# Kernel optimization log

Measured on AMD Instinct MI355X. Metric: run time of the kernel, lower is better.

Reference implementation:

```python
import jax, jax.numpy as jnp
import numpy as np

INV_L_MIN, INV_L_MAX = 0.5, 2.0

def _gelu(v):
    return jax.nn.gelu(v, approximate=False)  # torch F.gelu default = exact erf

def compute_gradient(f, directed_edges, edge_gradient_weights):
    # f: [b, c, n] ; directed_edges: [b, e, 2] (target, source) ; egw: [b, e, d]
    f = jnp.transpose(f, (0, 2, 1))                      # [b, n, c]
    b, n, c = f.shape
    e, d = edge_gradient_weights.shape[1], edge_gradient_weights.shape[2]
    target, source = directed_edges[..., 0], directed_edges[..., 1]
    fs = jnp.take_along_axis(f, source[:, :, None], axis=1)   # [b, e, c]
    ft = jnp.take_along_axis(f, target[:, :, None], axis=1)   # [b, e, c]
    # einsum('bed,bec->becd') then reshape -> channel-major (c*d) layout
    msg = (edge_gradient_weights[:, :, None, :] * (fs - ft)[:, :, :, None]).reshape(b, e, c * d)
    seg = (target + n * jnp.arange(b, dtype=target.dtype)[:, None]).reshape(-1)
    grad = jax.ops.segment_sum(msg.reshape(b * e, c * d), seg, num_segments=b * n)
    return jnp.transpose(grad.reshape(b, n, c * d), (0, 2, 1))  # [b, c*d, n]

def spectral_conv(x, wc, ws_, w0, bc, bs, b0, wbc, wbs, wb0):
    # x: [b, c, n]; bases: [b, n, k, w]; weights: [c, o, k, w]
    xc = jnp.einsum('bcx,bxkw->bckw', x, wbc)
    xs = jnp.einsum('bcx,bxkw->bckw', x, wbs)
    x0 = jnp.einsum('bcx,bxkw->bckw', x, wb0)
    fc = jnp.einsum('bckw,cokw->bokw', xc, wc) - jnp.einsum('bckw,cokw->bokw', xs, ws_)
    fs = jnp.einsum('bckw,cokw->bokw', xs, wc) + jnp.einsum('bckw,cokw->bokw', xc, ws_)
    f0 = jnp.einsum('bckw,cokw->bokw', x0, w0)
    return (jnp.einsum('bokw,bxkw->box', f0, b0)
            + 2 * jnp.einsum('bokw,bxkw->box', fc, bc)
            - 2 * jnp.einsum('bokw,bxkw->box', fs, bs))

def setup_inputs():
    key = jax.random.key(0)
    ks = jax.random.split(key, 16)
    B, N, E = 4, 20000, 100000
    NDIMS, NMEAS, NMODES = 3, 1, 32
    C, L = 128, 3
    IN_DIM, FC_DIM, OUT_DIM = 3, 128, 1
    f32 = jnp.float32
    inp = {}
    inp['x'] = jax.random.normal(ks[0], (B, N, IN_DIM), f32)
    inp['node_mask'] = jnp.ones((B, N, 1), jnp.int32)
    inp['nodes'] = jax.random.uniform(ks[1], (B, N, NDIMS), f32)
    inp['node_weights'] = jax.random.uniform(ks[2], (B, N, NMEAS), f32) / N
    inp['directed_edges'] = jax.random.randint(ks[3], (B, E, 2), 0, N, jnp.int32)
    inp['edge_gradient_weights'] = jax.random.normal(ks[4], (B, E, NDIMS), f32)
    # modes k = 2*pi*K/L0, K integer-like
    inp['modes'] = (2 * jnp.pi * jax.random.randint(ks[5], (NMODES, NDIMS, NMEAS), 1, 9)).astype(f32)
    # scaled_logit(1.0, 0.5, 2.0): sigmoid(l)=1/3 -> l=log(0.5)
    inp['inv_L_scale_latent'] = jnp.full((NDIMS, NMEAS), np.log(0.5), f32)
    inp['fc0_w'] = jax.random.normal(ks[6], (C, IN_DIM), f32) / np.sqrt(IN_DIM)
    inp['fc0_b'] = jnp.zeros((C,), f32)
    sc = 1.0 / (C * C)
    inp['swc'] = sc * jax.random.uniform(ks[7], (L, C, C, NMODES, NMEAS), f32)
    inp['sws'] = sc * jax.random.uniform(ks[8], (L, C, C, NMODES, NMEAS), f32)
    inp['sw0'] = sc * jax.random.uniform(ks[9], (L, C, C, 1, NMEAS), f32)
    inp['ww'] = jax.random.normal(ks[10], (L, C, C), f32) / np.sqrt(C)
    inp['wb'] = jnp.zeros((L, C), f32)
    inp['gw'] = jax.random.normal(ks[11], (L, C, NDIMS * C), f32) / np.sqrt(NDIMS * C)
    inp['gb'] = jnp.zeros((L, C), f32)
    inp['fc1_w'] = jax.random.normal(ks[12], (FC_DIM, C), f32) / np.sqrt(C)
    inp['fc1_b'] = jnp.zeros((FC_DIM,), f32)
    inp['fc2_w'] = jax.random.normal(ks[13], (OUT_DIM, FC_DIM), f32) / np.sqrt(FC_DIM)
    inp['fc2_b'] = jnp.zeros((OUT_DIM,), f32)
    return inp

def reference(x, node_mask, nodes, node_weights, directed_edges, edge_gradient_weights,
              modes, inv_L_scale_latent, fc0_w, fc0_b, swc, sws, sw0, ww, wb, gw, gb,
              fc1_w, fc1_b, fc2_w, fc2_b):
    inv_L = INV_L_MIN + (INV_L_MAX - INV_L_MIN) * jax.nn.sigmoid(inv_L_scale_latent)  # [d, w]
    t = jnp.einsum('bxd,kdw->bxkw', nodes, modes * inv_L[None])
    bc, bs = jnp.cos(t), jnp.sin(t)
    b0 = jnp.ones(t.shape[:2] + (1, t.shape[3]), t.dtype)
    w = node_weights[:, :, None, :]
    wbc, wbs, wb0 = bc * w, bs * w, b0 * w
    h = jnp.einsum('bni,ci->bnc', x, fc0_w) + fc0_b        # lift
    h = jnp.transpose(h, (0, 2, 1))                        # [b, C, n]
    L = swc.shape[0]
    for i in range(L):
        h1 = spectral_conv(h, swc[i], sws[i], sw0[i], bc, bs, b0, wbc, wbs, wb0)
        h2 = jnp.einsum('oc,bcn->bon', ww[i], h) + wb[i][None, :, None]
        g = compute_gradient(h, directed_edges, edge_gradient_weights)
        h3 = jnp.einsum('oc,bcn->bon', gw[i], g) + gb[i][None, :, None]
        h = h1 + h2 + h3
        if i != L - 1:
            h = _gelu(h)
    h = jnp.transpose(h, (0, 2, 1))                        # [b, n, C]
    h = _gelu(h @ fc1_w.T + fc1_b)
    return h @ fc2_w.T + fc2_b                             # [b, n, out_dim]
```

## Files before the change

### kernel.cpp

```cpp
#include <hip/hip_runtime.h>
#include <math.h>

#define B_ 4
#define N_ 20000
#define E_ 100000
#define C_ 128
#define K_ 32
#define NPAD 20480
#define NROWS (B_*N_ + 128)

typedef __attribute__((ext_vector_type(8))) short short8;
typedef __attribute__((ext_vector_type(4))) float floatx4;
typedef __attribute__((ext_vector_type(4))) unsigned int uintx4;
typedef __attribute__((ext_vector_type(2))) unsigned int uintx2;

__device__ __forceinline__ float gelu_exact(float x){
    return 0.5f * x * (1.0f + erff(x * 0.70710678118654752f));
}

__device__ __forceinline__ unsigned short f2bf(float f){
    unsigned int u = __builtin_bit_cast(unsigned int, f);
    u += 0x7FFFu + ((u >> 16) & 1u);
    return (unsigned short)(u >> 16);
}
__device__ __forceinline__ unsigned int pack2(float a, float b){
    return (unsigned int)f2bf(a) | ((unsigned int)f2bf(b) << 16);
}
__device__ __forceinline__ float bf2f(unsigned short u){
    unsigned int v = ((unsigned int)u) << 16;
    return __builtin_bit_cast(float, v);
}
__device__ __forceinline__ float u2f(unsigned int u){
    return __builtin_bit_cast(float, u);
}

#define WAITV(n) asm volatile("s_waitcnt vmcnt(" #n ")" ::: "memory")
#define BAR() __builtin_amdgcn_s_barrier()


__global__ __launch_bounds__(256) void basis_kernel(
    const float* __restrict__ nodes, const float* __restrict__ nw,
    const float* __restrict__ modes, const float* __restrict__ latent,
    unsigned short* __restrict__ bcb, unsigned short* __restrict__ bsb,
    unsigned short* __restrict__ wBt)
{
    __shared__ float lx[64], ly[64], lz[64], lwv[64];
    __shared__ unsigned short lTc[32*64], lTs[32*64];
    int b = blockIdx.y, n0 = blockIdx.x*64;
    int tid = threadIdx.x;
    size_t bN = (size_t)b*N_;
    if (tid < 64){
        int n = n0 + tid;
        float iL0 = 0.5f + 1.5f/(1.f+expf(-latent[0]));
        float iL1 = 0.5f + 1.5f/(1.f+expf(-latent[1]));
        float iL2 = 0.5f + 1.5f/(1.f+expf(-latent[2]));
        if (n < N_){
            lx[tid] = nodes[(bN+n)*3+0]*iL0;
            ly[tid] = nodes[(bN+n)*3+1]*iL1;
            lz[tid] = nodes[(bN+n)*3+2]*iL2;
            lwv[tid] = nw[bN+n];
        } else { lx[tid]=0.f; ly[tid]=0.f; lz[tid]=0.f; lwv[tid]=0.f; }
    }
    __syncthreads();
    int node = tid>>2, k0 = (tid&3)*8;
    float p0 = lx[node], p1 = ly[node], p2 = lz[node], w = lwv[node];
    float cv[8], sv[8];
    #pragma unroll
    for (int i=0;i<8;i++){
        int k = k0+i;
        float t = p0*modes[k*3+0] + p1*modes[k*3+1] + p2*modes[k*3+2];
        cv[i] = cosf(t); sv[i] = sinf(t);
        lTc[k*64 + node] = f2bf(w*cv[i]);
        lTs[k*64 + node] = f2bf(w*sv[i]);
    }
    int gn = n0 + node;
    if (gn < N_){
        uintx4 uc = (uintx4){pack2(cv[0],cv[1]), pack2(cv[2],cv[3]),
                             pack2(cv[4],cv[5]), pack2(cv[6],cv[7])};
        uintx4 us = (uintx4){pack2(sv[0],sv[1]), pack2(sv[2],sv[3]),
                             pack2(sv[4],sv[5]), pack2(sv[6],sv[7])};
        *(uintx4*)&bcb[(bN+gn)*K_ + k0] = uc;
        *(uintx4*)&bsb[(bN+gn)*K_ + k0] = us;
    }
    __syncthreads();
    #pragma unroll
    for (int i=0;i<5;i++){
        int idx = i*256 + tid;
        int row = idx>>4, seg = idx&15;
        unsigned short v0,v1,v2,v3;
        if (row < 32){
            v0=lTc[row*64+seg*4+0]; v1=lTc[row*64+seg*4+1];
            v2=lTc[row*64+seg*4+2]; v3=lTc[row*64+seg*4+3];
        } else if (row < 64){
            int r = row-32;
            v0=lTs[r*64+seg*4+0]; v1=lTs[r*64+seg*4+1];
            v2=lTs[r*64+seg*4+2]; v3=lTs[r*64+seg*4+3];
        } else if (row == 64){
            v0=f2bf(lwv[seg*4+0]); v1=f2bf(lwv[seg*4+1]);
            v2=f2bf(lwv[seg*4+2]); v3=f2bf(lwv[seg*4+3]);
        } else { v0=v1=v2=v3=0; }
        uintx2 u;
        u.x = (unsigned int)v0 | ((unsigned int)v1<<16);
        u.y = (unsigned int)v2 | ((unsigned int)v3<<16);
        *(uintx2*)&wBt[((size_t)b*80+row)*NPAD + n0 + seg*4] = u;
    }
}


__global__ __launch_bounds__(256) void fc0_kernel(
    const float* __restrict__ x, const float* __restrict__ w,
    const float* __restrict__ bvec, unsigned short* __restrict__ hN,
    unsigned short* __restrict__ hT)
{
    int idx = blockIdx.x*256 + threadIdx.x;
    if (idx >= B_*NPAD) return;
    int b = idx / NPAD, n = idx - b*NPAD;
    if (n >= N_){
        for (int c=0;c<C_;c++)
            hT[((size_t)b*C_+c)*NPAD + n] = 0;
        return;
    }
    size_t idn = (size_t)b*N_ + n;
    float x0 = x[idn*3+0], x1 = x[idn*3+1], x2 = x[idn*3+2];
    unsigned short* hr = hN + idn*C_;
    for (int c=0;c<C_;c+=4){
        float4 v;
        v.x = bvec[c+0] + x0*w[(c+0)*3] + x1*w[(c+0)*3+1] + x2*w[(c+0)*3+2];
        v.y = bvec[c+1] + x0*w[(c+1)*3] + x1*w[(c+1)*3+1] + x2*w[(c+1)*3+2];
        v.z = bvec[c+2] + x0*w[(c+2)*3] + x1*w[(c+2)*3+1] + x2*w[(c+2)*3+2];
        v.w = bvec[c+3] + x0*w[(c+3)*3] + x1*w[(c+3)*3+1] + x2*w[(c+3)*3+2];
        uintx2 u; u.x = pack2(v.x,v.y); u.y = pack2(v.z,v.w);
        *(uintx2*)(hr+c) = u;
        hT[((size_t)b*C_+c+0)*NPAD + n] = f2bf(v.x);
        hT[((size_t)b*C_+c+1)*NPAD + n] = f2bf(v.y);
        hT[((size_t)b*C_+c+2)*NPAD + n] = f2bf(v.z);
        hT[((size_t)b*C_+c+3)*NPAD + n] = f2bf(v.w);
    }
}


__global__ __launch_bounds__(256) void hist_kernel(
    const int* __restrict__ edges, int* __restrict__ cnt)
{
    int idx = blockIdx.x*256 + threadIdx.x;
    if (idx >= B_*E_) return;
    int b = idx / E_;
    int t = edges[(size_t)idx*2];
    atomicAdd(cnt + b*N_ + t, 1);
}

__global__ __launch_bounds__(1024) void scan_kernel(
    const int* __restrict__ cnt, int* __restrict__ rowptr, int* __restrict__ cur)
{
    __shared__ int wsum[16];
    int b = blockIdx.x, tid = threadIdx.x;
    int lane = tid & 63, wv = tid >> 6;
    const int CHUNK = 20;
    int start = tid * CHUNK;
    int lc[CHUNK];
    int lsum = 0;
    #pragma unroll
    for (int i=0;i<CHUNK;i++){
        int n = start + i;
        int v = (n < N_) ? cnt[b*N_+n] : 0;
        lc[i] = v; lsum += v;
    }
    int v = lsum;
    #pragma unroll
    for (int off=1; off<64; off<<=1){
        int t = __shfl_up(v, off, 64);
        if (lane >= off) v += t;
    }
    if (lane == 63) wsum[wv] = v;
    __syncthreads();
    if (wv == 0 && lane < 16){
        int wv2 = wsum[lane];
        #pragma unroll
        for (int off=1; off<16; off<<=1){
            int t = __shfl_up(wv2, off, 64);
            if (lane >= off) wv2 += t;
        }
        wsum[lane] = wv2;
    }
    __syncthreads();
    int waveoff = (wv == 0) ? 0 : wsum[wv-1];
    int excl = waveoff + v - lsum;
    #pragma unroll
    for (int i=0;i<CHUNK;i++){
        int n = start + i;
        if (n < N_){
            rowptr[b*(N_+1)+n] = excl;
            cur[b*N_+n] = excl;
            excl += lc[i];
        }
    }
    if (tid == 0) rowptr[b*(N_+1)+N_] = E_;
}

__global__ __launch_bounds__(256) void fill_kernel(
    const int* __restrict__ edges, const float* __restrict__ egw,
    int* __restrict__ cur, uintx4* __restrict__ epack)
{
    int idx = blockIdx.x*256 + threadIdx.x;
    if (idx >= B_*E_) return;
    int b = idx / E_;
    int t = edges[(size_t)idx*2];
    int src = edges[(size_t)idx*2+1];
    uintx4 rec;
    rec.x = (unsigned int)src;
    rec.y = __builtin_bit_cast(unsigned int, egw[(size_t)idx*3+0]);
    rec.z = __builtin_bit_cast(unsigned int, egw[(size_t)idx*3+1]);
    rec.w = __builtin_bit_cast(unsigned int, egw[(size_t)idx*3+2]);
    int pos = atomicAdd(cur + b*N_ + t, 1);
    epack[(size_t)b*E_ + pos] = rec;
}


__global__ __launch_bounds__(256) void wconv_kernel(
    const float* __restrict__ ww, const float* __restrict__ gw,
    unsigned short* __restrict__ wcat3)
{
    int o = blockIdx.x, l = blockIdx.y, t = threadIdx.x;
    const float* ww_l = ww + (size_t)l*C_*C_;
    const float* gw_l = gw + (size_t)l*C_*C_*3;
    int k = t*2;
    float a, bv;
    if (k < 128){ a = ww_l[(size_t)o*C_ + k];      bv = ww_l[(size_t)o*C_ + k + 1]; }
    else        { a = gw_l[(size_t)o*384 + k-128]; bv = gw_l[(size_t)o*384 + k-127]; }
    *(unsigned int*)&wcat3[((size_t)l*C_ + o)*512 + k] = pack2(a, bv);
}

__global__ __launch_bounds__(64) void fc1conv_kernel(
    const float* __restrict__ fc1w, unsigned short* __restrict__ w16)
{
    int o = blockIdx.x, t = threadIdx.x;
    int k = t*2;
    *(unsigned int*)&w16[(size_t)o*C_ + k] = pack2(fc1w[(size_t)o*C_+k], fc1w[(size_t)o*C_+k+1]);
}


__global__ __launch_bounds__(256) void stageA_kernel(
    const unsigned short* __restrict__ hT, const unsigned short* __restrict__ wBt,
    float* __restrict__ part)
{
    __shared__ unsigned short stg[2][160*64];
    int b = blockIdx.y;
    int blk = blockIdx.x >> 1;
    int half = blockIdx.x & 1;
    int tid = threadIdx.x;
    int wv = tid>>6, lane = tid&63, l15 = lane&15, quad = lane>>4;
    floatx4 acc[5];
    #pragma unroll
    for (int mt=0;mt<5;mt++) acc[mt]=(floatx4){0,0,0,0};
    size_t hbase = (size_t)b*C_*NPAD;
    size_t wbase = (size_t)b*80*NPAD;
    int n0 = blk*320;
    const unsigned short* sp[5];
    #pragma unroll
    for (int q=0;q<5;q++){
        int li = q*256 + tid;
        int r = li>>3;
        int u = (li&7) ^ (r&7);
        int rw = (r < 80) ? r : 79;
        sp[q] = (r < 96) ? (wBt + wbase + (size_t)rw*NPAD + n0 + u*8)
                         : (hT  + hbase + (size_t)(half*64 + r-96)*NPAD + n0 + u*8);
    }

#define SSTG(ch) do{ \
    _Pragma("unroll") \
    for (int q=0;q<5;q++) \
        __builtin_amdgcn_global_load_lds( \
            (const __attribute__((address_space(1))) void*)(sp[q] + (ch)*64), \
            (__attribute__((address_space(3))) void*)&stg[(ch)&1][q*2048 + wv*512], \
            16, 0, 0); }while(0)

#define SCOMP(ch) do{ \
    __builtin_amdgcn_s_setprio(1); \
    _Pragma("unroll") \
    for (int ks=0; ks<2; ks++){ \
        short8 bfrag = *(const short8*)&stg[(ch)&1][(96 + wv*16 + l15)*64 + (((ks*4+quad)^(l15&7))*8)]; \
        _Pragma("unroll") \
        for (int mt=0;mt<5;mt++){ \
            short8 af = *(const short8*)&stg[(ch)&1][(mt*16+l15)*64 + (((ks*4+quad)^(l15&7))*8)]; \
            acc[mt] = __builtin_amdgcn_mfma_f32_16x16x32_bf16(af, bfrag, acc[mt], 0,0,0); \
        } } \
    __builtin_amdgcn_s_setprio(0); }while(0)

    SSTG(0); SSTG(1);
    WAITV(5); BAR(); SCOMP(0); BAR(); SSTG(2);
    WAITV(5); BAR(); SCOMP(1); BAR(); SSTG(3);
    WAITV(5); BAR(); SCOMP(2); BAR(); SSTG(4);
    WAITV(5); BAR(); SCOMP(3);
    WAITV(0); BAR(); SCOMP(4);
#undef SSTG
#undef SCOMP

    float* pblk = part + ((size_t)(b*64+blk))*80*C_;
    int cg = half*64 + wv*16 + l15;
    #pragma unroll
    for (int mt=0;mt<5;mt++){
        #pragma unroll
        for (int r=0;r<4;r++){
            int kcol = mt*16 + quad*4 + r;
            pblk[kcol*C_ + cg] = acc[mt][r];
        }
    }
}

__global__ __launch_bounds__(256) void reducePart_kernel(
    const float* __restrict__ part, float* __restrict__ xq)
{
    int idx = blockIdx.x*256 + threadIdx.x;
    if (idx >= B_*80*C_) return;
    int b = idx / (80*C_);
    int r = idx - b*80*C_;
    float s = 0.f;
    #pragma unroll 8
    for (int blk=0; blk<64; blk++)
        s += part[((size_t)(b*64+blk))*80*C_ + r];
    xq[idx] = s;
}


__global__ __launch_bounds__(256) void mix_kernel(
    const float* __restrict__ xq, const float* __restrict__ swc_l,
    const float* __restrict__ sws_l, const float* __restrict__ sw0_l,
    unsigned short* __restrict__ wfb, float* __restrict__ f0)
{
    __shared__ float s64[4][64];
    int o = blockIdx.x, tid = threadIdx.x;
    int b = tid >> 6, t = tid & 63;
    int k = t & 31; bool isS = t >= 32;
    const float* xqb = xq + (size_t)b*80*C_;
    float acc = 0.f;
    for (int c=0;c<C_;c++){
        float xc = xqb[k*C_ + c], xs = xqb[(32+k)*C_ + c];
        float wc = swc_l[((size_t)c*C_+o)*K_ + k];
        float ws = sws_l[((size_t)c*C_+o)*K_ + k];
        acc += isS ? (xs*wc + xc*ws) : (xc*wc - xs*ws);
    }
    wfb[((size_t)b*C_+o)*64 + t] = f2bf(isS ? -2.f*acc : 2.f*acc);
    float p = xqb[64*C_ + t]      * sw0_l[(size_t)t*C_+o]
            + xqb[64*C_ + 64 + t] * sw0_l[(size_t)(t+64)*C_+o];
    s64[b][t] = p; __syncthreads();
    if (t==0){
        float s=0.f;
        for (int i=0;i<64;i++) s += s64[b][i];
        f0[b*C_+o] = s;
    }
}


__global__ __launch_bounds__(256) void grad_kernel(
    const unsigned short* __restrict__ hN, const uintx4* __restrict__ epack,
    const int* __restrict__ rowptr, unsigned short* __restrict__ g)
{
    int flat = blockIdx.x;
    int xcd = flat & 7;
    int b = xcd >> 1;
    int grp = (flat >> 3)*2 + (xcd & 1);
    int n = grp*4 + (threadIdx.x >> 6);
    int cp = threadIdx.x & 63;
    size_t bN = (size_t)b*N_;
    size_t bE = (size_t)b*E_;
    int r0 = rowptr[b*(N_+1)+n], r1 = rowptr[b*(N_+1)+n+1];
    unsigned int hcu = *(const unsigned int*)&hN[(bN+n)*C_ + cp*2];
    float hc0 = bf2f((unsigned short)hcu), hc1 = bf2f((unsigned short)(hcu>>16));
    float a00=0.f,a01=0.f,a02=0.f, a10=0.f,a11=0.f,a12=0.f;
    int i = r0;
    for (; i + 3 < r1; i += 4){
        uintx4 p0 = epack[bE + i];
        uintx4 p1 = epack[bE + i + 1];
        uintx4 p2 = epack[bE + i + 2];
        uintx4 p3 = epack[bE + i + 3];
        unsigned int u0 = *(const unsigned int*)&hN[(bN+(int)p0.x)*C_ + cp*2];
        unsigned int u1 = *(const unsigned int*)&hN[(bN+(int)p1.x)*C_ + cp*2];
        unsigned int u2 = *(const unsigned int*)&hN[(bN+(int)p2.x)*C_ + cp*2];
        unsigned int u3 = *(const unsigned int*)&hN[(bN+(int)p3.x)*C_ + cp*2];
        float d00 = bf2f((unsigned short)u0) - hc0, d01 = bf2f((unsigned short)(u0>>16)) - hc1;
        float d10 = bf2f((unsigned short)u1) - hc0, d11 = bf2f((unsigned short)(u1>>16)) - hc1;
        float d20 = bf2f((unsigned short)u2) - hc0, d21 = bf2f((unsigned short)(u2>>16)) - hc1;
        float d30 = bf2f((unsigned short)u3) - hc0, d31 = bf2f((unsigned short)(u3>>16)) - hc1;
        a00 += u2f(p0.y)*d00; a01 += u2f(p0.z)*d00; a02 += u2f(p0.w)*d00;
        a10 += u2f(p0.y)*d01; a11 += u2f(p0.z)*d01; a12 += u2f(p0.w)*d01;
        a00 += u2f(p1.y)*d10; a01 += u2f(p1.z)*d10; a02 += u2f(p1.w)*d10;
        a10 += u2f(p1.y)*d11; a11 += u2f(p1.z)*d11; a12 += u2f(p1.w)*d11;
        a00 += u2f(p2.y)*d20; a01 += u2f(p2.z)*d20; a02 += u2f(p2.w)*d20;
        a10 += u2f(p2.y)*d21; a11 += u2f(p2.z)*d21; a12 += u2f(p2.w)*d21;
        a00 += u2f(p3.y)*d30; a01 += u2f(p3.z)*d30; a02 += u2f(p3.w)*d30;
        a10 += u2f(p3.y)*d31; a11 += u2f(p3.z)*d31; a12 += u2f(p3.w)*d31;
    }
    for (; i < r1; ++i){
        uintx4 p0 = epack[bE + i];
        unsigned int u0 = *(const unsigned int*)&hN[(bN+(int)p0.x)*C_ + cp*2];
        float w00 = u2f(p0.y), w01 = u2f(p0.z), w02 = u2f(p0.w);
        float d00 = bf2f((unsigned short)u0) - hc0;
        float d01 = bf2f((unsigned short)(u0>>16)) - hc1;
        a00 += w00*d00; a01 += w01*d00; a02 += w02*d00;
        a10 += w00*d01; a11 += w01*d01; a12 += w02*d01;
    }
    unsigned short* gr = g + (bN+n)*(size_t)384 + cp*6;
    *(unsigned int*)(gr+0) = pack2(a00,a01);
    *(unsigned int*)(gr+2) = pack2(a02,a10);
    *(unsigned int*)(gr+4) = pack2(a11,a12);
}


__global__ __launch_bounds__(256) void gemm_kernel(
    const unsigned short* __restrict__ hN, const unsigned short* __restrict__ g,
    const unsigned short* __restrict__ bcb, const unsigned short* __restrict__ bsb,
    const unsigned short* __restrict__ wcat, const unsigned short* __restrict__ wfb,
    const float* __restrict__ wb_l, const float* __restrict__ gb_l,
    const float* __restrict__ f0,
    unsigned short* __restrict__ hNo, unsigned short* __restrict__ hT, int apply_gelu)
{
    __shared__ unsigned short As4[4][4096];
    int b = blockIdx.y;
    int nb0 = blockIdx.x*64;
    int tid = threadIdx.x;
    int wv = tid>>6, lane = tid&63, l15 = lane&15, quad = lane>>4;
    floatx4 acc[4][2];
    #pragma unroll
    for (int mt=0;mt<4;mt++)
        #pragma unroll
        for (int ot=0;ot<2;ot++) acc[mt][ot] = (floatx4){0.f,0.f,0.f,0.f};
    size_t bN = (size_t)b*N_;

    const unsigned short* sh[2]; const unsigned short* sg[2]; const unsigned short* sb[2];
    #pragma unroll
    for (int q=0;q<2;q++){
        int li = q*256 + tid;
        int row = li>>3, col = (li&7) ^ (row&7);
        size_t gr = bN + (size_t)(nb0 + row);
        sh[q] = hN + gr*C_  + col*8;
        sg[q] = g  + gr*384 + col*8;
        sb[q] = (col < 4) ? (bcb + gr*K_ + col*8) : (bsb + gr*K_ + (col-4)*8);
    }
    int o0 = wv*32 + l15, o1 = o0 + 16;
    const unsigned short* w0p = wcat + (size_t)o0*512 + quad*8;
    const unsigned short* w1p = wcat + (size_t)o1*512 + quad*8;
    const unsigned short* fb0 = wfb + ((size_t)b*C_ + o0)*64 + quad*8;
    const unsigned short* fb1 = wfb + ((size_t)b*C_ + o1)*64 + quad*8;

    short8 bb[3][2][2];

#define LOADB(ch) do{ \
    if ((ch) < 8){ \
        bb[(ch)%3][0][0] = *(const short8*)(w0p + (ch)*64); \
        bb[(ch)%3][0][1] = *(const short8*)(w0p + (ch)*64 + 32); \
        bb[(ch)%3][1][0] = *(const short8*)(w1p + (ch)*64); \
        bb[(ch)%3][1][1] = *(const short8*)(w1p + (ch)*64 + 32); \
    } else { \
        bb[(ch)%3][0][0] = *(const short8*)(fb0); \
        bb[(ch)%3][0][1] = *(const short8*)(fb0 + 32); \
        bb[(ch)%3][1][0] = *(const short8*)(fb1); \
        bb[(ch)%3][1][1] = *(const short8*)(fb1 + 32); \
    } }while(0)

#define STAGE1(ch,q) \
    __builtin_amdgcn_global_load_lds( \
        (const __attribute__((address_space(1))) void*)( \
            ((ch) < 2) ? (sh[q] + (ch)*64) : \
            ((ch) < 8) ? (sg[q] + ((ch)-2)*64) : sb[q] ), \
        (__attribute__((address_space(3))) void*)&As4[(ch)&3][(q)*2048 + wv*512], \
        16, 0, 0)
#define STAGE(ch) do{ STAGE1(ch,0); STAGE1(ch,1); }while(0)

#define COMPUTE(ch) do{ \
    __builtin_amdgcn_s_setprio(1); \
    _Pragma("unroll") \
    for (int ks=0; ks<2; ks++){ \
        _Pragma("unroll") \
        for (int mt=0; mt<4; mt++){ \
            short8 af = *(const short8*)&As4[(ch)&3][(mt*16+l15)*64 + (((ks*4+quad)^(l15&7))*8)]; \
            acc[mt][0] = __builtin_amdgcn_mfma_f32_16x16x32_bf16(af, bb[(ch)%3][0][ks], acc[mt][0], 0,0,0); \
            acc[mt][1] = __builtin_amdgcn_mfma_f32_16x16x32_bf16(af, bb[(ch)%3][1][ks], acc[mt][1], 0,0,0); \
        } } \
    __builtin_amdgcn_s_setprio(0); }while(0)

    LOADB(0); LOADB(1);
    STAGE(0); STAGE(1); STAGE(2);
    WAITV(4); BAR(); LOADB(2); STAGE(3); COMPUTE(0);
    WAITV(8); BAR(); LOADB(3); STAGE(4); COMPUTE(1);
    WAITV(8); BAR(); LOADB(4); STAGE(5); COMPUTE(2);
    WAITV(8); BAR(); LOADB(5); STAGE(6); COMPUTE(3);
    WAITV(8); BAR(); LOADB(6); STAGE(7); COMPUTE(4);
    WAITV(8); BAR(); LOADB(7); STAGE(8); COMPUTE(5);
    WAITV(8); BAR(); LOADB(8);           COMPUTE(6);
    WAITV(6); BAR();                     COMPUTE(7);
    WAITV(0); BAR();                     COMPUTE(8);

#undef LOADB
#undef STAGE1
#undef STAGE
#undef COMPUTE

    float biasv[2]; int oo[2];
    oo[0]=o0; oo[1]=o1;
    #pragma unroll
    for (int ot=0;ot<2;ot++)
        biasv[ot] = wb_l[oo[ot]] + gb_l[oo[ot]] + f0[(size_t)b*C_ + oo[ot]];
    unsigned short* AsF = &As4[0][0];
    if (apply_gelu) __syncthreads();
    #pragma unroll
    for (int mt=0;mt<4;mt++){
        #pragma unroll
        for (int ot=0;ot<2;ot++){
            int nb = nb0 + mt*16 + quad*4;
            float v4[4];
            #pragma unroll
            for (int r=0;r<4;r++){
                float vv = acc[mt][ot][r] + biasv[ot];
                if (apply_gelu) vv = gelu_exact(vv);
                bool ok = (nb + r < N_);
                if (ok) hNo[(bN+nb+r)*C_ + oo[ot]] = f2bf(vv);
                v4[r] = ok ? vv : 0.f;
            }
            if (apply_gelu){
                uintx2 u; u.x = pack2(v4[0],v4[1]); u.y = pack2(v4[2],v4[3]);
                *(uintx2*)&AsF[oo[ot]*72 + mt*16 + quad*4] = u;
            }
        }
    }
    if (apply_gelu){
        __syncthreads();
        int orow = tid>>1, half = tid&1;
        uintx4 u0 = *(const uintx4*)&AsF[orow*72 + half*32];
        uintx4 u1 = *(const uintx4*)&AsF[orow*72 + half*32 + 8];
        unsigned short* dst = &hT[((size_t)b*C_ + orow)*NPAD + nb0 + half*32];
        *(uintx4*)dst       = u0;
        *(uintx4*)(dst + 8) = u1;
    }
}


__global__ __launch_bounds__(256) void final_kernel(
    const unsigned short* __restrict__ hN, const unsigned short* __restrict__ fc1b16,
    const float* __restrict__ fc1b, const float* __restrict__ fc2w,
    const float* __restrict__ fc2b, float* __restrict__ out)
{
    __shared__ unsigned short As[64*72];
    __shared__ float pp[4*64];
    int b = blockIdx.y;
    int nb0 = blockIdx.x*64;
    int tid = threadIdx.x;
    int a_n = tid>>2, a_s = tid&3;
    int wv = tid>>6, lane = tid&63, l15 = lane&15, quad = lane>>4;
    floatx4 acc[4][2];
    #pragma unroll
    for (int mt=0;mt<4;mt++){ acc[mt][0]=(floatx4){0,0,0,0}; acc[mt][1]=(floatx4){0,0,0,0}; }
    size_t bN = (size_t)b*N_;
    int gn = nb0 + a_n; bool av = gn < N_;
    size_t row = bN + (size_t)(av ? gn : 0);
    const unsigned short* hrow = hN + row*C_;
    int o0 = wv*32 + l15, o1 = o0 + 16;
    const unsigned short* w0p = fc1b16 + (size_t)o0*C_ + quad*8;
    const unsigned short* w1p = fc1b16 + (size_t)o1*C_ + quad*8;

    for (int ch=0; ch<2; ++ch){
        uintx4 v0 = (uintx4){0,0,0,0}, v1 = (uintx4){0,0,0,0};
        if (av){
            const uintx4* pptr = (const uintx4*)(hrow + ch*64 + a_s*16);
            v0 = pptr[0]; v1 = pptr[1];
        }
        *(uintx4*)&As[a_n*72 + a_s*16]     = v0;
        *(uintx4*)&As[a_n*72 + a_s*16 + 8] = v1;
        __syncthreads();
        #pragma unroll
        for (int ks=0; ks<2; ks++){
            short8 bfr0 = *(const short8*)(w0p + ch*64 + ks*32);
            short8 bfr1 = *(const short8*)(w1p + ch*64 + ks*32);
            #pragma unroll
            for (int mt=0; mt<4; mt++){
                short8 af = *(const short8*)&As[(mt*16+l15)*72 + ks*32 + quad*8];
                acc[mt][0] = __builtin_amdgcn_mfma_f32_16x16x32_bf16(af, bfr0, acc[mt][0], 0,0,0);
                acc[mt][1] = __builtin_amdgcn_mfma_f32_16x16x32_bf16(af, bfr1, acc[mt][1], 0,0,0);
            }
        }
        __syncthreads();
    }
    float fw0 = fc2w[o0], fw1 = fc2w[o1];
    float b0 = fc1b[o0], b1 = fc1b[o1];
    #pragma unroll
    for (int mt=0;mt<4;mt++){
        float s[4];
        #pragma unroll
        for (int r=0;r<4;r++)
            s[r] = fw0*gelu_exact(acc[mt][0][r] + b0) + fw1*gelu_exact(acc[mt][1][r] + b1);
        #pragma unroll
        for (int m=1;m<16;m<<=1)
            #pragma unroll
            for (int r=0;r<4;r++)
                s[r] += __shfl_xor(s[r], m, 16);
        if (l15 < 4){
            float v = (l15==0)?s[0]:(l15==1)?s[1]:(l15==2)?s[2]:s[3];
            pp[wv*64 + mt*16 + quad*4 + l15] = v;
        }
    }
    __syncthreads();
    if (tid < 64){
        float sum = pp[tid] + pp[64+tid] + pp[128+tid] + pp[192+tid] + fc2b[0];
        int n = nb0 + tid;
        if (n < N_) out[bN + n] = sum;
    }
}


extern "C" void kernel_launch(void* const* d_in, const int* in_sizes, int n_in,
                              void* d_out, int out_size, void* d_ws, size_t ws_size,
                              hipStream_t stream)
{
    const float* x      = (const float*)d_in[0];
    const float* nodes  = (const float*)d_in[2];
    const float* nw     = (const float*)d_in[3];
    const int*   edges  = (const int*)  d_in[4];
    const float* egw    = (const float*)d_in[5];
    const float* modes  = (const float*)d_in[6];
    const float* latent = (const float*)d_in[7];
    const float* fc0w   = (const float*)d_in[8];
    const float* fc0b   = (const float*)d_in[9];
    const float* swc    = (const float*)d_in[10];
    const float* sws    = (const float*)d_in[11];
    const float* sw0    = (const float*)d_in[12];
    const float* ww     = (const float*)d_in[13];
    const float* wb     = (const float*)d_in[14];
    const float* gw     = (const float*)d_in[15];
    const float* gb     = (const float*)d_in[16];
    const float* fc1w   = (const float*)d_in[17];
    const float* fc1b   = (const float*)d_in[18];
    const float* fc2w   = (const float*)d_in[19];
    const float* fc2b   = (const float*)d_in[20];
    float* out = (float*)d_out;

    char* W = (char*)d_ws;
    size_t off = 0;
    unsigned short* bcB = (unsigned short*)(W+off); off += (size_t)NROWS*K_*2;
    unsigned short* bsB = (unsigned short*)(W+off); off += (size_t)NROWS*K_*2;
    unsigned short* wBt = (unsigned short*)(W+off); off += (size_t)B_*80*NPAD*2;
    unsigned short* hT  = (unsigned short*)(W+off); off += (size_t)B_*C_*NPAD*2;
    unsigned short* hNa = (unsigned short*)(W+off); off += (size_t)NROWS*C_*2;
    unsigned short* hNb = (unsigned short*)(W+off); off += (size_t)NROWS*C_*2;
    unsigned short* g   = (unsigned short*)(W+off); off += (size_t)NROWS*C_*3*2;
    unsigned short* wcat3=(unsigned short*)(W+off); off += (size_t)3*C_*512*2;
    unsigned short* wfb = (unsigned short*)(W+off); off += (size_t)B_*C_*64*2;
    unsigned short* fcw16=(unsigned short*)(W+off); off += (size_t)C_*C_*2;
    float* part = (float*)(W+off); off += (size_t)B_*64*80*C_*4;
    float* xq   = (float*)(W+off); off += (size_t)B_*80*C_*4;
    float* f0   = (float*)(W+off); off += (size_t)B_*C_*4;
    off = (off + 15) & ~(size_t)15;
    uintx4* epack = (uintx4*)(W+off); off += (size_t)B_*E_*16;
    int* cnt    = (int*)(W+off); off += (size_t)B_*N_*4;
    int* rowptr = (int*)(W+off); off += (size_t)B_*(N_+1)*4 + 16;
    int* cur    = (int*)(W+off); off += (size_t)B_*N_*4;

    (void)hipMemsetAsync(cnt, 0, (size_t)B_*N_*sizeof(int), stream);
    basis_kernel<<<dim3(NPAD/64, B_), 256, 0, stream>>>(
        nodes, nw, modes, latent, bcB, bsB, wBt);
    fc0_kernel  <<<(B_*NPAD+255)/256, 256, 0, stream>>>(x, fc0w, fc0b, hNa, hT);
    hist_kernel <<<(B_*E_+255)/256, 256, 0, stream>>>(edges, cnt);
    scan_kernel <<<B_, 1024, 0, stream>>>(cnt, rowptr, cur);
    fill_kernel <<<(B_*E_+255)/256, 256, 0, stream>>>(edges, egw, cur, epack);
    wconv_kernel<<<dim3(C_,3), 256, 0, stream>>>(ww, gw, wcat3);
    fc1conv_kernel<<<C_, 64, 0, stream>>>(fc1w, fcw16);

    unsigned short* hc = hNa; unsigned short* hn = hNb;
    for (int l=0; l<3; ++l){
        stageA_kernel<<<dim3(128,B_), 256, 0, stream>>>(hT, wBt, part);
        reducePart_kernel<<<(B_*80*C_+255)/256, 256, 0, stream>>>(part, xq);
        mix_kernel<<<C_, 256, 0, stream>>>(
            xq, swc + (size_t)l*C_*C_*K_, sws + (size_t)l*C_*C_*K_,
            sw0 + (size_t)l*C_*C_, wfb, f0);
        grad_kernel<<<N_, 256, 0, stream>>>(hc, epack, rowptr, g);
        gemm_kernel<<<dim3((N_+63)/64,B_), 256, 0, stream>>>(
            hc, g, bcB, bsB, wcat3 + (size_t)l*C_*512, wfb,
            wb + (size_t)l*C_, gb + (size_t)l*C_,
            f0, hn, hT, (l<2) ? 1 : 0);
        unsigned short* t = hc; hc = hn; hn = t;
    }
    final_kernel<<<dim3((N_+63)/64,B_), 256, 0, stream>>>(
        hc, fcw16, fc1b, fc2w, fc2b, out);
}
```

Baseline: 529.2 us.

## Drop MFMA setprio, transpose xq for mix, async-stage final kernel loads

Removes s_setprio bracketing around the MFMA loops in the stageA and gemm kernels. Stores the reduced spectral coefficients transposed so the mix kernel reads them contiguously per lane. The mix kernel now runs one 64-thread wave per (o,b) and reduces f0 with wave shuffles instead of shared memory. The final kernel stages activations via global_load_lds into a swizzled LDS buffer without row bounds checks, relying on buffer padding.

Measured after the change: 517.4 us. 2.2% less time.

```diff
diff --git a/kernel.cpp b/kernel.cpp
--- a/kernel.cpp
+++ b/kernel.cpp
@@ -275,7 +275,6 @@
             16, 0, 0); }while(0)
 
 #define SCOMP(ch) do{ \
-    __builtin_amdgcn_s_setprio(1); \
     _Pragma("unroll") \
     for (int ks=0; ks<2; ks++){ \
         short8 bfrag = *(const short8*)&stg[(ch)&1][(96 + wv*16 + l15)*64 + (((ks*4+quad)^(l15&7))*8)]; \
@@ -283,8 +282,7 @@
         for (int mt=0;mt<5;mt++){ \
             short8 af = *(const short8*)&stg[(ch)&1][(mt*16+l15)*64 + (((ks*4+quad)^(l15&7))*8)]; \
             acc[mt] = __builtin_amdgcn_mfma_f32_16x16x32_bf16(af, bfrag, acc[mt], 0,0,0); \
-        } } \
-    __builtin_amdgcn_s_setprio(0); }while(0)
+        } } }while(0)
 
     SSTG(0); SSTG(1);
     WAITV(5); BAR(); SCOMP(0); BAR(); SSTG(2);
@@ -308,46 +306,45 @@
 }
 
 __global__ __launch_bounds__(256) void reducePart_kernel(
-    const float* __restrict__ part, float* __restrict__ xq)
+    const float* __restrict__ part, float* __restrict__ xqT)
 {
     int idx = blockIdx.x*256 + threadIdx.x;
     if (idx >= B_*80*C_) return;
     int b = idx / (80*C_);
     int r = idx - b*80*C_;
+    int kcol = r >> 7, c = r & 127;
     float s = 0.f;
     #pragma unroll 8
     for (int blk=0; blk<64; blk++)
         s += part[((size_t)(b*64+blk))*80*C_ + r];
-    xq[idx] = s;
-}
-
-
-__global__ __launch_bounds__(256) void mix_kernel(
-    const float* __restrict__ xq, const float* __restrict__ swc_l,
+    xqT[(size_t)b*80*C_ + c*80 + kcol] = s;
+}
+
+
+__global__ __launch_bounds__(64) void mix_kernel(
+    const float* __restrict__ xqT, const float* __restrict__ swc_l,
     const float* __restrict__ sws_l, const float* __restrict__ sw0_l,
     unsigned short* __restrict__ wfb, float* __restrict__ f0)
 {
-    __shared__ float s64[4][64];
-    int o = blockIdx.x, tid = threadIdx.x;
-    int b = tid >> 6, t = tid & 63;
+    int o = blockIdx.x, b = blockIdx.y;
+    int t = threadIdx.x;
     int k = t & 31; bool isS = t >= 32;
-    const float* xqb = xq + (size_t)b*80*C_;
+    const float* xqb = xqT + (size_t)b*80*C_;
     float acc = 0.f;
+    #pragma unroll 4
     for (int c=0;c<C_;c++){
-        float xc = xqb[k*C_ + c], xs = xqb[(32+k)*C_ + c];
+        float xc = xqb[c*80 + k];
+        float xs = xqb[c*80 + 32 + k];
         float wc = swc_l[((size_t)c*C_+o)*K_ + k];
         float ws = sws_l[((size_t)c*C_+o)*K_ + k];
         acc += isS ? (xs*wc + xc*ws) : (xc*wc - xs*ws);
     }
     wfb[((size_t)b*C_+o)*64 + t] = f2bf(isS ? -2.f*acc : 2.f*acc);
-    float p = xqb[64*C_ + t]      * sw0_l[(size_t)t*C_+o]
-            + xqb[64*C_ + 64 + t] * sw0_l[(size_t)(t+64)*C_+o];
-    s64[b][t] = p; __syncthreads();
-    if (t==0){
-        float s=0.f;
-        for (int i=0;i<64;i++) s += s64[b][i];
-        f0[b*C_+o] = s;
-    }
+    float p = xqb[t*80 + 64]        * sw0_l[(size_t)t*C_+o]
+            + xqb[(t+64)*80 + 64]   * sw0_l[(size_t)(t+64)*C_+o];
+    #pragma unroll
+    for (int m=1;m<64;m<<=1) p += __shfl_xor(p, m, 64);
+    if (t==0) f0[(size_t)b*C_+o] = p;
 }
 
 
@@ -467,7 +464,6 @@
 #define STAGE(ch) do{ STAGE1(ch,0); STAGE1(ch,1); }while(0)
 
 #define COMPUTE(ch) do{ \
-    __builtin_amdgcn_s_setprio(1); \
     _Pragma("unroll") \
     for (int ks=0; ks<2; ks++){ \
         _Pragma("unroll") \
@@ -475,8 +471,7 @@
             short8 af = *(const short8*)&As4[(ch)&3][(mt*16+l15)*64 + (((ks*4+quad)^(l15&7))*8)]; \
             acc[mt][0] = __builtin_amdgcn_mfma_f32_16x16x32_bf16(af, bb[(ch)%3][0][ks], acc[mt][0], 0,0,0); \
             acc[mt][1] = __builtin_amdgcn_mfma_f32_16x16x32_bf16(af, bb[(ch)%3][1][ks], acc[mt][1], 0,0,0); \
-        } } \
-    __builtin_amdgcn_s_setprio(0); }while(0)
+        } } }while(0)
 
     LOADB(0); LOADB(1);
     STAGE(0); STAGE(1); STAGE(2);
@@ -539,46 +534,53 @@
     const float* __restrict__ fc1b, const float* __restrict__ fc2w,
     const float* __restrict__ fc2b, float* __restrict__ out)
 {
-    __shared__ unsigned short As[64*72];
+    __shared__ unsigned short Fs[2][4096];
     __shared__ float pp[4*64];
     int b = blockIdx.y;
     int nb0 = blockIdx.x*64;
     int tid = threadIdx.x;
-    int a_n = tid>>2, a_s = tid&3;
     int wv = tid>>6, lane = tid&63, l15 = lane&15, quad = lane>>4;
     floatx4 acc[4][2];
     #pragma unroll
     for (int mt=0;mt<4;mt++){ acc[mt][0]=(floatx4){0,0,0,0}; acc[mt][1]=(floatx4){0,0,0,0}; }
     size_t bN = (size_t)b*N_;
-    int gn = nb0 + a_n; bool av = gn < N_;
-    size_t row = bN + (size_t)(av ? gn : 0);
-    const unsigned short* hrow = hN + row*C_;
+    const unsigned short* sfp[2];
+    #pragma unroll
+    for (int q=0;q<2;q++){
+        int li = q*256 + tid;
+        int row = li>>3, u = (li&7) ^ (row&7);
+        sfp[q] = hN + (bN + (size_t)(nb0 + row))*C_ + u*8;
+    }
     int o0 = wv*32 + l15, o1 = o0 + 16;
     const unsigned short* w0p = fc1b16 + (size_t)o0*C_ + quad*8;
     const unsigned short* w1p = fc1b16 + (size_t)o1*C_ + quad*8;
 
-    for (int ch=0; ch<2; ++ch){
-        uintx4 v0 = (uintx4){0,0,0,0}, v1 = (uintx4){0,0,0,0};
-        if (av){
-            const uintx4* pptr = (const uintx4*)(hrow + ch*64 + a_s*16);
-            v0 = pptr[0]; v1 = pptr[1];
-        }
-        *(uintx4*)&As[a_n*72 + a_s*16]     = v0;
-        *(uintx4*)&As[a_n*72 + a_s*16 + 8] = v1;
-        __syncthreads();
-        #pragma unroll
-        for (int ks=0; ks<2; ks++){
-            short8 bfr0 = *(const short8*)(w0p + ch*64 + ks*32);
-            short8 bfr1 = *(const short8*)(w1p + ch*64 + ks*32);
-            #pragma unroll
-            for (int mt=0; mt<4; mt++){
-                short8 af = *(const short8*)&As[(mt*16+l15)*72 + ks*32 + quad*8];
-                acc[mt][0] = __builtin_amdgcn_mfma_f32_16x16x32_bf16(af, bfr0, acc[mt][0], 0,0,0);
-                acc[mt][1] = __builtin_amdgcn_mfma_f32_16x16x32_bf16(af, bfr1, acc[mt][1], 0,0,0);
-            }
-        }
-        __syncthreads();
-    }
+#define FSTG(ch) do{ \
+    _Pragma("unroll") \
+    for (int q=0;q<2;q++) \
+        __builtin_amdgcn_global_load_lds( \
+            (const __attribute__((address_space(1))) void*)(sfp[q] + (ch)*64), \
+            (__attribute__((address_space(3))) void*)&Fs[ch][q*2048 + wv*512], \
+            16, 0, 0); }while(0)
+
+#define FCOMP(ch) do{ \
+    _Pragma("unroll") \
+    for (int ks=0; ks<2; ks++){ \
+        short8 bfr0 = *(const short8*)(w0p + (ch)*64 + ks*32); \
+        short8 bfr1 = *(const short8*)(w1p + (ch)*64 + ks*32); \
+        _Pragma("unroll") \
+        for (int mt=0; mt<4; mt++){ \
+            short8 af = *(const short8*)&Fs[ch][(mt*16+l15)*64 + (((ks*4+quad)^(l15&7))*8)]; \
+            acc[mt][0] = __builtin_amdgcn_mfma_f32_16x16x32_bf16(af, bfr0, acc[mt][0], 0,0,0); \
+            acc[mt][1] = __builtin_amdgcn_mfma_f32_16x16x32_bf16(af, bfr1, acc[mt][1], 0,0,0); \
+        } } }while(0)
+
+    FSTG(0); FSTG(1);
+    WAITV(2); BAR(); FCOMP(0);
+    WAITV(0); BAR(); FCOMP(1);
+#undef FSTG
+#undef FCOMP
+
     float fw0 = fc2w[o0], fw1 = fc2w[o1];
     float b0 = fc1b[o0], b1 = fc1b[o1];
     #pragma unroll
@@ -667,7 +669,7 @@
     for (int l=0; l<3; ++l){
         stageA_kernel<<<dim3(128,B_), 256, 0, stream>>>(hT, wBt, part);
         reducePart_kernel<<<(B_*80*C_+255)/256, 256, 0, stream>>>(part, xq);
-        mix_kernel<<<C_, 256, 0, stream>>>(
+        mix_kernel<<<dim3(C_,B_), 64, 0, stream>>>(
             xq, swc + (size_t)l*C_*C_*K_, sws + (size_t)l*C_*C_*K_,
             sw0 + (size_t)l*C_*C_, wfb, f0);
         grad_kernel<<<N_, 256, 0, stream>>>(hc, epack, rowptr, g);
```
